# Kernel tuning notes

Measured on AMD Instinct MI355X. Metric: run time of the kernel, lower is better.

## Reference

```python
import jax, jax.numpy as jnp
import numpy as np

ALPHA = 1.0
DIAG_FILL = 500000.0


def _batch_pairwise_dist(x, y):
    # x: [B, Nx, D], y: [B, Ny, D] -> squared-distance matrix [B, Nx, Ny]
    xx = jnp.sum(x * x, axis=-1)  # [B, Nx]
    yy = jnp.sum(y * y, axis=-1)  # [B, Ny]
    zz = jnp.einsum('bnd,bmd->bnm', x, y)  # [B, Nx, Ny]
    return xx[:, :, None] + yy[:, None, :] - 2.0 * zz


def setup_inputs() -> dict:
    key = jax.random.key(0)
    k1, k2 = jax.random.split(key)
    B, N, D = 4, 4096, 3
    gts = jax.random.normal(k1, (B, N, D), dtype=jnp.float32)
    preds = jax.random.normal(k2, (B, N, D), dtype=jnp.float32)
    return {"gts": gts, "preds": preds}


def reference(gts, preds):
    # Cross-term Chamfer: P[b,i,j] = ||gts_i - preds_j||^2
    P = _batch_pairwise_dist(gts, preds)  # [B, Ng, Np]
    loss_1 = jnp.sum(jnp.min(P, axis=1), axis=1)  # min over gts, sum over preds
    loss_2 = jnp.sum(jnp.min(P, axis=2), axis=1)  # min over preds, sum over gts

    # Self nearest-neighbor distance distributions (diagonal masked out)
    Ng = gts.shape[1]
    Np = preds.shape[1]
    eye_g = jnp.eye(Ng, dtype=bool)
    eye_p = jnp.eye(Np, dtype=bool)
    P1 = jnp.where(eye_g[None, :, :], DIAG_FILL, _batch_pairwise_dist(gts, gts))
    P2 = jnp.where(eye_p[None, :, :], DIAG_FILL, _batch_pairwise_dist(preds, preds))

    mins1 = jnp.sort(jnp.min(P1, axis=1), axis=1)  # [B, Ng]
    mins2 = jnp.sort(jnp.min(P2, axis=1), axis=1)  # [B, Np]
    min_ps = min(mins1.shape[1], mins2.shape[1])
    loss_ordering = jnp.sum((mins1[:, :min_ps] - mins2[:, :min_ps]) ** 2, axis=1)

    return loss_1 + loss_2 + ALPHA * loss_ordering
```

## Files before the change

### kernel.cpp

```cpp
#include <hip/hip_runtime.h>

constexpr int BATCH = 4;
constexpr int NPTS  = 4096;
constexpr int QC    = 1024;
constexpr int TC    = 512;
constexpr int NTHR  = 256;
constexpr int QPT   = QC / NTHR;
constexpr int PADN  = NPTS + (NPTS >> 4);


__global__ __launch_bounds__(NTHR) void nn_pass(const float* __restrict__ gts,
                                                const float* __restrict__ preds,
                                                unsigned int* __restrict__ nnmin) {
    const int pass  = blockIdx.z & 3;
    const int b     = blockIdx.z >> 2;
    const int qbase = blockIdx.y * QC;
    const int tbase = blockIdx.x * TC;
    const bool selfp = (pass >= 2);
    const float* __restrict__ A = (pass == 0 || pass == 2) ? gts : preds;
    const float* __restrict__ T = (pass == 1 || pass == 2) ? gts : preds;

    __shared__ float4 tp[TC];
    for (int k = threadIdx.x; k < TC; k += NTHR) {
        const float* p = T + ((size_t)b * NPTS + tbase + k) * 3;
        tp[k] = make_float4(p[0], p[1], p[2], 0.f);
    }
    __syncthreads();

    float qx[QPT], qy[QPT], qz[QPT], mn[QPT];
    int qidx[QPT];
#pragma unroll
    for (int q = 0; q < QPT; ++q) {
        const int qi = qbase + threadIdx.x + q * NTHR;
        qidx[q] = qi;
        const float* p = A + ((size_t)b * NPTS + qi) * 3;
        qx[q] = p[0]; qy[q] = p[1]; qz[q] = p[2];
        mn[q] = 1e30f;
    }

    if (selfp) {
#pragma unroll 4
        for (int j = 0; j < TC; ++j) {
            const float4 t = tp[j];
            const int tj = tbase + j;
#pragma unroll
            for (int q = 0; q < QPT; ++q) {
                const float dx = qx[q] - t.x, dy = qy[q] - t.y, dz = qz[q] - t.z;
                float d = dx * dx;
                d = fmaf(dy, dy, d);
                d = fmaf(dz, dz, d);
                d = (tj == qidx[q]) ? 1e30f : d;
                mn[q] = fminf(mn[q], d);
            }
        }
    } else {
#pragma unroll 4
        for (int j = 0; j < TC; ++j) {
            const float4 t = tp[j];
#pragma unroll
            for (int q = 0; q < QPT; ++q) {
                const float dx = qx[q] - t.x, dy = qy[q] - t.y, dz = qz[q] - t.z;
                float d = dx * dx;
                d = fmaf(dy, dy, d);
                d = fmaf(dz, dz, d);
                mn[q] = fminf(mn[q], d);
            }
        }
    }

    unsigned int* dst = nnmin + ((size_t)pass * BATCH + b) * NPTS;
#pragma unroll
    for (int q = 0; q < QPT; ++q)
        atomicMin(&dst[qidx[q]], __float_as_uint(mn[q]));
}


template<int K, int J>
__device__ __forceinline__ void bstep(float (&v)[16], const int t, float* __restrict__ sbuf) {
    if constexpr (J >= 1024) {
        const bool asc = ((t & (K >> 4)) == 0);
        const bool keepmin = (((t & (J >> 4)) == 0) == asc);
        const int tp = t ^ (J >> 4);
#pragma unroll
        for (int e = 0; e < 16; ++e) sbuf[17 * t + e] = v[e];
        __syncthreads();
#pragma unroll
        for (int e = 0; e < 16; ++e) {
            const float pv = sbuf[17 * tp + e];
            v[e] = keepmin ? fminf(v[e], pv) : fmaxf(v[e], pv);
        }
        __syncthreads();
    } else if constexpr (J >= 16) {
        constexpr int lm = J >> 4;
        const bool asc = ((t & (K >> 4)) == 0);
        const bool keepmin = (((t & lm) == 0) == asc);
#pragma unroll
        for (int e = 0; e < 16; ++e) {
            const float pv = __shfl_xor(v[e], lm, 64);
            v[e] = keepmin ? fminf(v[e], pv) : fmaxf(v[e], pv);
        }
    } else {
#pragma unroll
        for (int e = 0; e < 16; ++e) {
            if ((e & J) == 0) {
                const int p = e | J;
                bool asc;
                if constexpr (K >= 16) asc = ((t & (K >> 4)) == 0);
                else                   asc = ((e & K) == 0);
                const float a = v[e], c = v[p];
                v[e] = asc ? fminf(a, c) : fmaxf(a, c);
                v[p] = asc ? fmaxf(a, c) : fminf(a, c);
            }
        }
    }
}

template<int K, int J>
__device__ __forceinline__ void bseq(float (&v)[16], const int t, float* __restrict__ sbuf) {
    bstep<K, J>(v, t, sbuf);
    if constexpr (J > 1) bseq<K, (J >> 1)>(v, t, sbuf);
}

template<int K>
__device__ __forceinline__ void bsortk(float (&v)[16], const int t, float* __restrict__ sbuf) {
    bseq<K, (K >> 1)>(v, t, sbuf);
    if constexpr (K < NPTS) bsortk<(K << 1)>(v, t, sbuf);
}

__global__ __launch_bounds__(512) void nn_final(const unsigned int* __restrict__ nnmin,
                                                float* __restrict__ out) {
    const int b   = blockIdx.x;
    const int tid = threadIdx.x;
    const int g   = tid >> 8;
    const int t   = tid & 255;
    __shared__ float s[2][PADN];
    __shared__ float red[512];
    float* sbuf = s[g];

    const unsigned int* src = nnmin + ((size_t)(2 + g) * BATCH + b) * NPTS;
    float v[16];
#pragma unroll
    for (int q = 0; q < 4; ++q) {
        const uint4 u = reinterpret_cast<const uint4*>(src)[t * 4 + q];
        v[q * 4 + 0] = __uint_as_float(u.x);
        v[q * 4 + 1] = __uint_as_float(u.y);
        v[q * 4 + 2] = __uint_as_float(u.z);
        v[q * 4 + 3] = __uint_as_float(u.w);
    }

    bsortk<2>(v, t, sbuf);

#pragma unroll
    for (int e = 0; e < 16; ++e) sbuf[17 * t + e] = v[e];
    __syncthreads();

    float part = 0.f;
    const float* m0 = (const float*)(nnmin + ((size_t)0 * BATCH + b) * NPTS);
    const float* m1 = (const float*)(nnmin + ((size_t)1 * BATCH + b) * NPTS);
#pragma unroll
    for (int q = 0; q < 2; ++q) {
        const float4 u0 = reinterpret_cast<const float4*>(m0)[tid + 512 * q];
        const float4 u1 = reinterpret_cast<const float4*>(m1)[tid + 512 * q];
        part += u0.x + u0.y + u0.z + u0.w + u1.x + u1.y + u1.z + u1.w;
    }
#pragma unroll
    for (int e = 0; e < 8; ++e) {
        const int i  = tid + 512 * e;
        const int pi = i + (i >> 4);
        const float d = s[0][pi] - s[1][pi];
        part = fmaf(d, d, part);
    }

    red[tid] = part;
    __syncthreads();
    for (int sh = 256; sh > 0; sh >>= 1) {
        if (tid < sh) red[tid] += red[tid + sh];
        __syncthreads();
    }
    if (tid == 0) out[b] = red[0];
}

extern "C" void kernel_launch(void* const* d_in, const int* in_sizes, int n_in,
                              void* d_out, int out_size, void* d_ws, size_t ws_size,
                              hipStream_t stream) {
    const float* gts   = (const float*)d_in[0];
    const float* preds = (const float*)d_in[1];
    float* out = (float*)d_out;
    unsigned int* nnmin = (unsigned int*)d_ws;

    hipMemsetAsync(d_ws, 0x7F, (size_t)4 * BATCH * NPTS * sizeof(unsigned int), stream);
    dim3 grid(NPTS / TC, NPTS / QC, BATCH * 4);
    nn_pass<<<grid, NTHR, 0, stream>>>(gts, preds, nnmin);
    nn_final<<<BATCH, 512, 0, stream>>>(nnmin, out);
}
```

Before: 123.0 us.

## Fuse memset, NN pass and final reduction into one cooperative kernel

Replaces the memset plus two kernel launches with a single cooperative kernel that initializes the min buffer, runs the nearest-neighbour pass, then sorts and reduces, separated by grid-wide syncs. The sort is split across 8 blocks (one per self-pass and batch) instead of 4 blocks each handling two sorts, and the distance is rewritten as |q|^2+|t|^2-2q·t using precomputed norms in the float4 w slot. The aim is to remove launch overhead and shorten the inner-loop arithmetic, at the cost of grid-sync latency and a requirement that all 512 blocks be co-resident. The norm-expansion form can change rounding compared with the direct difference form.

```diff
diff --git a/kernel.cpp b/kernel.cpp
--- a/kernel.cpp
+++ b/kernel.cpp
@@ -1,4 +1,7 @@
 #include <hip/hip_runtime.h>
+#include <hip/hip_cooperative_groups.h>
+
+namespace cg = cooperative_groups;
 
 constexpr int BATCH = 4;
 constexpr int NPTS  = 4096;
@@ -7,72 +10,7 @@
 constexpr int NTHR  = 256;
 constexpr int QPT   = QC / NTHR;
 constexpr int PADN  = NPTS + (NPTS >> 4);
-
-
-__global__ __launch_bounds__(NTHR) void nn_pass(const float* __restrict__ gts,
-                                                const float* __restrict__ preds,
-                                                unsigned int* __restrict__ nnmin) {
-    const int pass  = blockIdx.z & 3;
-    const int b     = blockIdx.z >> 2;
-    const int qbase = blockIdx.y * QC;
-    const int tbase = blockIdx.x * TC;
-    const bool selfp = (pass >= 2);
-    const float* __restrict__ A = (pass == 0 || pass == 2) ? gts : preds;
-    const float* __restrict__ T = (pass == 1 || pass == 2) ? gts : preds;
-
-    __shared__ float4 tp[TC];
-    for (int k = threadIdx.x; k < TC; k += NTHR) {
-        const float* p = T + ((size_t)b * NPTS + tbase + k) * 3;
-        tp[k] = make_float4(p[0], p[1], p[2], 0.f);
-    }
-    __syncthreads();
-
-    float qx[QPT], qy[QPT], qz[QPT], mn[QPT];
-    int qidx[QPT];
-#pragma unroll
-    for (int q = 0; q < QPT; ++q) {
-        const int qi = qbase + threadIdx.x + q * NTHR;
-        qidx[q] = qi;
-        const float* p = A + ((size_t)b * NPTS + qi) * 3;
-        qx[q] = p[0]; qy[q] = p[1]; qz[q] = p[2];
-        mn[q] = 1e30f;
-    }
-
-    if (selfp) {
-#pragma unroll 4
-        for (int j = 0; j < TC; ++j) {
-            const float4 t = tp[j];
-            const int tj = tbase + j;
-#pragma unroll
-            for (int q = 0; q < QPT; ++q) {
-                const float dx = qx[q] - t.x, dy = qy[q] - t.y, dz = qz[q] - t.z;
-                float d = dx * dx;
-                d = fmaf(dy, dy, d);
-                d = fmaf(dz, dz, d);
-                d = (tj == qidx[q]) ? 1e30f : d;
-                mn[q] = fminf(mn[q], d);
-            }
-        }
-    } else {
-#pragma unroll 4
-        for (int j = 0; j < TC; ++j) {
-            const float4 t = tp[j];
-#pragma unroll
-            for (int q = 0; q < QPT; ++q) {
-                const float dx = qx[q] - t.x, dy = qy[q] - t.y, dz = qz[q] - t.z;
-                float d = dx * dx;
-                d = fmaf(dy, dy, d);
-                d = fmaf(dz, dz, d);
-                mn[q] = fminf(mn[q], d);
-            }
-        }
-    }
-
-    unsigned int* dst = nnmin + ((size_t)pass * BATCH + b) * NPTS;
-#pragma unroll
-    for (int q = 0; q < QPT; ++q)
-        atomicMin(&dst[qidx[q]], __float_as_uint(mn[q]));
-}
+constexpr int NNTOT = 4 * BATCH * NPTS;
 
 
 template<int K, int J>
@@ -127,57 +65,146 @@
     if constexpr (K < NPTS) bsortk<(K << 1)>(v, t, sbuf);
 }
 
-__global__ __launch_bounds__(512) void nn_final(const unsigned int* __restrict__ nnmin,
-                                                float* __restrict__ out) {
-    const int b   = blockIdx.x;
+__global__ __launch_bounds__(NTHR) void chamfer_all(const float* __restrict__ gts,
+                                                    const float* __restrict__ preds,
+                                                    unsigned int* __restrict__ nnmin,
+                                                    float* __restrict__ cross,
+                                                    float* __restrict__ out) {
     const int tid = threadIdx.x;
-    const int g   = tid >> 8;
-    const int t   = tid & 255;
-    __shared__ float s[2][PADN];
-    __shared__ float red[512];
-    float* sbuf = s[g];
-
-    const unsigned int* src = nnmin + ((size_t)(2 + g) * BATCH + b) * NPTS;
-    float v[16];
-#pragma unroll
-    for (int q = 0; q < 4; ++q) {
-        const uint4 u = reinterpret_cast<const uint4*>(src)[t * 4 + q];
-        v[q * 4 + 0] = __uint_as_float(u.x);
-        v[q * 4 + 1] = __uint_as_float(u.y);
-        v[q * 4 + 2] = __uint_as_float(u.z);
-        v[q * 4 + 3] = __uint_as_float(u.w);
-    }
-
-    bsortk<2>(v, t, sbuf);
-
-#pragma unroll
-    for (int e = 0; e < 16; ++e) sbuf[17 * t + e] = v[e];
-    __syncthreads();
-
-    float part = 0.f;
-    const float* m0 = (const float*)(nnmin + ((size_t)0 * BATCH + b) * NPTS);
-    const float* m1 = (const float*)(nnmin + ((size_t)1 * BATCH + b) * NPTS);
-#pragma unroll
-    for (int q = 0; q < 2; ++q) {
-        const float4 u0 = reinterpret_cast<const float4*>(m0)[tid + 512 * q];
-        const float4 u1 = reinterpret_cast<const float4*>(m1)[tid + 512 * q];
-        part += u0.x + u0.y + u0.z + u0.w + u1.x + u1.y + u1.z + u1.w;
-    }
-#pragma unroll
-    for (int e = 0; e < 8; ++e) {
-        const int i  = tid + 512 * e;
-        const int pi = i + (i >> 4);
-        const float d = s[0][pi] - s[1][pi];
-        part = fmaf(d, d, part);
-    }
-
-    red[tid] = part;
-    __syncthreads();
-    for (int sh = 256; sh > 0; sh >>= 1) {
-        if (tid < sh) red[tid] += red[tid + sh];
-        __syncthreads();
-    }
-    if (tid == 0) out[b] = red[0];
+    const int bid = blockIdx.x + gridDim.x * (blockIdx.y + gridDim.y * blockIdx.z);
+    __shared__ __align__(16) float smem[PADN];
+    float4* tp = reinterpret_cast<float4*>(smem);
+
+    {
+        const int flat = bid * NTHR + tid;
+        if (flat < NNTOT) nnmin[flat] = 0x7F800000u;
+    }
+    __threadfence();
+    cg::this_grid().sync();
+
+    {
+        const int pass  = blockIdx.z & 3;
+        const int b     = blockIdx.z >> 2;
+        const int qbase = blockIdx.y * QC;
+        const int tbase = blockIdx.x * TC;
+        const bool selfp = (pass >= 2);
+        const float* __restrict__ A = (pass == 0 || pass == 2) ? gts : preds;
+        const float* __restrict__ T = (pass == 1 || pass == 2) ? gts : preds;
+
+        for (int k = tid; k < TC; k += NTHR) {
+            const float* p = T + ((size_t)b * NPTS + tbase + k) * 3;
+            const float x = p[0], y = p[1], z = p[2];
+            tp[k] = make_float4(x, y, z, fmaf(x, x, fmaf(y, y, z * z)));
+        }
+        __syncthreads();
+
+        float qx[QPT], qy[QPT], qz[QPT], qa[QPT], mn[QPT];
+        int qidx[QPT];
+#pragma unroll
+        for (int q = 0; q < QPT; ++q) {
+            const int qi = qbase + tid + q * NTHR;
+            qidx[q] = qi;
+            const float* p = A + ((size_t)b * NPTS + qi) * 3;
+            qx[q] = p[0]; qy[q] = p[1]; qz[q] = p[2];
+            qa[q] = fmaf(qx[q], qx[q], fmaf(qy[q], qy[q], qz[q] * qz[q]));
+            mn[q] = 1e30f;
+        }
+
+        if (selfp) {
+#pragma unroll 4
+            for (int j = 0; j < TC; ++j) {
+                const float4 t = tp[j];
+                const int tj = tbase + j;
+#pragma unroll
+                for (int q = 0; q < QPT; ++q) {
+                    float dot = qx[q] * t.x;
+                    dot = fmaf(qy[q], t.y, dot);
+                    dot = fmaf(qz[q], t.z, dot);
+                    float d = fmaf(-2.f, dot, qa[q] + t.w);
+                    d = (tj == qidx[q]) ? 1e30f : d;
+                    mn[q] = fminf(mn[q], d);
+                }
+            }
+        } else {
+#pragma unroll 4
+            for (int j = 0; j < TC; ++j) {
+                const float4 t = tp[j];
+#pragma unroll
+                for (int q = 0; q < QPT; ++q) {
+                    float dot = qx[q] * t.x;
+                    dot = fmaf(qy[q], t.y, dot);
+                    dot = fmaf(qz[q], t.z, dot);
+                    const float d = fmaf(-2.f, dot, qa[q] + t.w);
+                    mn[q] = fminf(mn[q], d);
+                }
+            }
+        }
+
+        unsigned int* dst = nnmin + ((size_t)pass * BATCH + b) * NPTS;
+#pragma unroll
+        for (int q = 0; q < QPT; ++q)
+            atomicMin(&dst[qidx[q]], __float_as_uint(mn[q]));
+    }
+    __threadfence();
+    cg::this_grid().sync();
+
+    if (bid < 16) {
+        const int s = bid & 3, b = bid >> 2;
+        float* slot = reinterpret_cast<float*>(nnmin) + ((size_t)s * BATCH + b) * NPTS;
+        if (s < 2) {
+            float acc = 0.f;
+#pragma unroll
+            for (int q = 0; q < 4; ++q) {
+                const float4 u = reinterpret_cast<const float4*>(slot)[tid * 4 + q];
+                acc += u.x + u.y + u.z + u.w;
+            }
+#pragma unroll
+            for (int sh = 1; sh <= 32; sh <<= 1) acc += __shfl_xor(acc, sh, 64);
+            if ((tid & 63) == 0) smem[tid >> 6] = acc;
+            __syncthreads();
+            if (tid == 0) cross[bid] = smem[0] + smem[1] + smem[2] + smem[3];
+        } else {
+            float v[16];
+#pragma unroll
+            for (int q = 0; q < 4; ++q) {
+                const float4 u = reinterpret_cast<const float4*>(slot)[tid * 4 + q];
+                v[q * 4 + 0] = u.x; v[q * 4 + 1] = u.y;
+                v[q * 4 + 2] = u.z; v[q * 4 + 3] = u.w;
+            }
+            bsortk<2>(v, tid, smem);
+#pragma unroll
+            for (int q = 0; q < 4; ++q)
+                reinterpret_cast<float4*>(slot)[tid * 4 + q] =
+                    make_float4(v[q * 4 + 0], v[q * 4 + 1], v[q * 4 + 2], v[q * 4 + 3]);
+        }
+    }
+    __threadfence();
+    cg::this_grid().sync();
+
+    if (bid < BATCH) {
+        const int b = bid;
+        const float* s2 = reinterpret_cast<const float*>(nnmin) + ((size_t)2 * BATCH + b) * NPTS;
+        const float* s3 = reinterpret_cast<const float*>(nnmin) + ((size_t)3 * BATCH + b) * NPTS;
+        float acc = 0.f;
+#pragma unroll
+        for (int q = 0; q < 4; ++q) {
+            const float4 a = reinterpret_cast<const float4*>(s2)[tid * 4 + q];
+            const float4 c = reinterpret_cast<const float4*>(s3)[tid * 4 + q];
+            float d;
+            d = a.x - c.x; acc = fmaf(d, d, acc);
+            d = a.y - c.y; acc = fmaf(d, d, acc);
+            d = a.z - c.z; acc = fmaf(d, d, acc);
+            d = a.w - c.w; acc = fmaf(d, d, acc);
+        }
+#pragma unroll
+        for (int sh = 1; sh <= 32; sh <<= 1) acc += __shfl_xor(acc, sh, 64);
+        __syncthreads();
+        if ((tid & 63) == 0) smem[tid >> 6] = acc;
+        __syncthreads();
+        if (tid == 0)
+            out[b] = smem[0] + smem[1] + smem[2] + smem[3]
+                   + cross[4 * b] + cross[4 * b + 1];
+    }
 }
 
 extern "C" void kernel_launch(void* const* d_in, const int* in_sizes, int n_in,
@@ -187,9 +214,10 @@
     const float* preds = (const float*)d_in[1];
     float* out = (float*)d_out;
     unsigned int* nnmin = (unsigned int*)d_ws;
-
-    hipMemsetAsync(d_ws, 0x7F, (size_t)4 * BATCH * NPTS * sizeof(unsigned int), stream);
-    dim3 grid(NPTS / TC, NPTS / QC, BATCH * 4);
-    nn_pass<<<grid, NTHR, 0, stream>>>(gts, preds, nnmin);
-    nn_final<<<BATCH, 512, 0, stream>>>(nnmin, out);
-}
+    float* cross = (float*)((char*)d_ws + NNTOT * sizeof(unsigned int));
+
+    void* args[] = {(void*)&gts, (void*)&preds, (void*)&nnmin, (void*)&cross, (void*)&out};
+    hipLaunchCooperativeKernel((const void*)chamfer_all,
+                               dim3(NPTS / TC, NPTS / QC, BATCH * 4),
+                               dim3(NTHR), args, 0, stream);
+}
```

After: 333.3 us. +171.0%, slower.

## Expand squared distance via precomputed norms and double queries per thread

Applied to the files above, without the earlier changes.

Each pairwise distance is now computed as |t|^2 + |q|^2 - 2 q·t. Target norms are stored in the unused w lane of the shared-memory float4, and the query points are pre-scaled by -2, so the inner loop needs one add and three FMAs instead of three subtracts, a multiply and two FMAs. The query chunk per block doubles, giving eight queries per thread. That adds instruction-level parallelism and halves the number of target-tile loads per query, but it also halves the grid size and raises register use. The expanded form can produce slightly negative distances from rounding. Those then compare wrongly under the unsigned atomicMin.

```diff
diff --git a/kernel.cpp b/kernel.cpp
--- a/kernel.cpp
+++ b/kernel.cpp
@@ -2,7 +2,7 @@
 
 constexpr int BATCH = 4;
 constexpr int NPTS  = 4096;
-constexpr int QC    = 1024;
+constexpr int QC    = 2048;
 constexpr int TC    = 512;
 constexpr int NTHR  = 256;
 constexpr int QPT   = QC / NTHR;
@@ -23,18 +23,21 @@
     __shared__ float4 tp[TC];
     for (int k = threadIdx.x; k < TC; k += NTHR) {
         const float* p = T + ((size_t)b * NPTS + tbase + k) * 3;
-        tp[k] = make_float4(p[0], p[1], p[2], 0.f);
+        const float x = p[0], y = p[1], z = p[2];
+        tp[k] = make_float4(x, y, z, fmaf(x, x, fmaf(y, y, z * z)));
     }
     __syncthreads();
 
-    float qx[QPT], qy[QPT], qz[QPT], mn[QPT];
-    int qidx[QPT];
+    float m2x[QPT], m2y[QPT], m2z[QPT], qa[QPT], mn[QPT];
+    int dj[QPT];
 #pragma unroll
     for (int q = 0; q < QPT; ++q) {
         const int qi = qbase + threadIdx.x + q * NTHR;
-        qidx[q] = qi;
+        dj[q] = qi - tbase;
         const float* p = A + ((size_t)b * NPTS + qi) * 3;
-        qx[q] = p[0]; qy[q] = p[1]; qz[q] = p[2];
+        const float x = p[0], y = p[1], z = p[2];
+        m2x[q] = -2.f * x; m2y[q] = -2.f * y; m2z[q] = -2.f * z;
+        qa[q] = fmaf(x, x, fmaf(y, y, z * z));
         mn[q] = 1e30f;
     }
 
@@ -42,14 +45,13 @@
 #pragma unroll 4
         for (int j = 0; j < TC; ++j) {
             const float4 t = tp[j];
-            const int tj = tbase + j;
 #pragma unroll
             for (int q = 0; q < QPT; ++q) {
-                const float dx = qx[q] - t.x, dy = qy[q] - t.y, dz = qz[q] - t.z;
-                float d = dx * dx;
-                d = fmaf(dy, dy, d);
-                d = fmaf(dz, dz, d);
-                d = (tj == qidx[q]) ? 1e30f : d;
+                float d = t.w + qa[q];
+                d = fmaf(m2x[q], t.x, d);
+                d = fmaf(m2y[q], t.y, d);
+                d = fmaf(m2z[q], t.z, d);
+                d = (j == dj[q]) ? 1e30f : d;
                 mn[q] = fminf(mn[q], d);
             }
         }
@@ -59,10 +61,10 @@
             const float4 t = tp[j];
 #pragma unroll
             for (int q = 0; q < QPT; ++q) {
-                const float dx = qx[q] - t.x, dy = qy[q] - t.y, dz = qz[q] - t.z;
-                float d = dx * dx;
-                d = fmaf(dy, dy, d);
-                d = fmaf(dz, dz, d);
+                float d = t.w + qa[q];
+                d = fmaf(m2x[q], t.x, d);
+                d = fmaf(m2y[q], t.y, d);
+                d = fmaf(m2z[q], t.z, d);
                 mn[q] = fminf(mn[q], d);
             }
         }
@@ -71,9 +73,8 @@
     unsigned int* dst = nnmin + ((size_t)pass * BATCH + b) * NPTS;
 #pragma unroll
     for (int q = 0; q < QPT; ++q)
-        atomicMin(&dst[qidx[q]], __float_as_uint(mn[q]));
+        atomicMin(&dst[qbase + threadIdx.x + q * NTHR], __float_as_uint(mn[q]));
 }
-
 
 template<int K, int J>
 __device__ __forceinline__ void bstep(float (&v)[16], const int t, float* __restrict__ sbuf) {
```

Result: slower. 135.2 us (+10.0%).
